# Kernel tuning notes

Measured on AMD Instinct MI355X. Metric: run time of the kernel, lower is better.

## Reference

```python
import jax, jax.numpy as jnp
import numpy as np

EMBED_DIM = 1024
NUM_HEADS = 16
HEAD_DIM = EMBED_DIM // NUM_HEADS


def setup_inputs() -> dict:
    key = jax.random.key(0)
    k_x, k_wqkv, k_bqkv, k_wo, k_bo = jax.random.split(key, 5)
    B, T, C = 4, 2048, EMBED_DIM
    bound = 1.0 / np.sqrt(C)
    return {
        "x": jax.random.normal(k_x, (B, T, C), dtype=jnp.float32),
        "w_qkv": jax.random.uniform(k_wqkv, (C, 3 * C), jnp.float32, -bound, bound),
        "b_qkv": jax.random.uniform(k_bqkv, (3 * C,), jnp.float32, -bound, bound),
        "w_out": jax.random.uniform(k_wo, (C, C), jnp.float32, -bound, bound),
        "b_out": jax.random.uniform(k_bo, (C,), jnp.float32, -bound, bound),
    }


def reference(x, w_qkv, b_qkv, w_out, b_out):
    B, T, C = x.shape
    H, D = NUM_HEADS, HEAD_DIM
    qkv = x @ w_qkv + b_qkv                       # [B,T,3C]
    qkv = qkv.reshape(B, T, 3, H, D)
    q, k, v = qkv[:, :, 0], qkv[:, :, 1], qkv[:, :, 2]  # [B,T,H,D]
    scale = 1.0 / np.sqrt(D).astype(np.float32)
    scores = jnp.einsum("bqhd,bkhd->bhqk", q, k) * scale  # [B,H,T,T]
    causal = jnp.tril(jnp.ones((T, T), dtype=bool))
    scores = jnp.where(causal, scores, -jnp.inf)
    attn = jax.nn.softmax(scores, axis=-1)
    # dropout p=0.0 / eval mode -> identity
    ctx = jnp.einsum("bhqk,bkhd->bqhd", attn, v).reshape(B, T, C)
    return ctx @ w_out + b_out
```

## Files before the change

kernel.cpp:

```cpp
#include <hip/hip_runtime.h>
#include <hip/hip_bf16.h>

#define NB 4
#define NT 2048
#define NC 1024
#define NH 16
#define ND 64
#define BT (NB*NT)
#define LOG2E 1.4426950408889634f
#define NEG_BIG (-3.0e38f)
#define MLC 28.853900817779268f

typedef __attribute__((ext_vector_type(8))) short bf16x8;
typedef __attribute__((ext_vector_type(4))) float f32x4;

static __device__ __forceinline__ short f2bf(float f) {
    union { float f; unsigned u; } v; v.f = f;
    unsigned r = (v.u + 0x7fffu + ((v.u >> 16) & 1u)) >> 16;
    return (short)r;
}

static __device__ __forceinline__ unsigned pk2(float a, float b) {
#if __has_builtin(__builtin_amdgcn_cvt_pk_bf16_f32)
    auto v = __builtin_amdgcn_cvt_pk_bf16_f32(a, b);
    union { decltype(v) v; unsigned u; } c; c.v = v; return c.u;
#else
    return (unsigned)(unsigned short)f2bf(a) | ((unsigned)(unsigned short)f2bf(b) << 16);
#endif
}

static __device__ __forceinline__ f32x4 mfma16(bf16x8 a, bf16x8 b, f32x4 c) {
    return __builtin_amdgcn_mfma_f32_16x16x32_bf16(a, b, c, 0, 0, 0);
}

static __device__ __forceinline__ float fexp2(float x) {
#if __has_builtin(__builtin_amdgcn_exp2f)
    return __builtin_amdgcn_exp2f(x);
#else
    return exp2f(x);
#endif
}

template<int GOFF>
static __device__ __forceinline__ void gload_lds16(const short* g, short* l) {
    __builtin_amdgcn_global_load_lds(
        (const __attribute__((address_space(1))) void*)g,
        (__attribute__((address_space(3))) void*)l,
        16, GOFF, 0);
}

__global__ __launch_bounds__(256)
void xcvt(const float* __restrict__ x, short* __restrict__ xb)
{
    const size_t i = ((size_t)blockIdx.x * 256 + threadIdx.x) * 8;
    float4 f0 = *(const float4*)(x + i);
    float4 f1 = *(const float4*)(x + i + 4);
    uint4 p;
    p.x = pk2(f0.x, f0.y); p.y = pk2(f0.z, f0.w);
    p.z = pk2(f1.x, f1.y); p.w = pk2(f1.z, f1.w);
    *(uint4*)(xb + i) = p;
}

__global__ __launch_bounds__(256)
void transpose_w(const float* __restrict__ w, short* __restrict__ wt, int R, int Cn)
{
    __shared__ short t[64][72];
    const int tid = threadIdx.x;
    const int r0 = blockIdx.x * 64;
    const int c0 = blockIdx.y * 64;
    {
        const int rl = tid >> 2, c4 = (tid & 3) << 4;
        const float* src = w + (size_t)(r0 + rl) * Cn + c0 + c4;
        float4 f0 = *(const float4*)(src + 0);
        float4 f1 = *(const float4*)(src + 4);
        float4 f2 = *(const float4*)(src + 8);
        float4 f3 = *(const float4*)(src + 12);
        short* d = &t[rl][c4];
        d[0]=f2bf(f0.x); d[1]=f2bf(f0.y); d[2]=f2bf(f0.z); d[3]=f2bf(f0.w);
        d[4]=f2bf(f1.x); d[5]=f2bf(f1.y); d[6]=f2bf(f1.z); d[7]=f2bf(f1.w);
        d[8]=f2bf(f2.x); d[9]=f2bf(f2.y); d[10]=f2bf(f2.z); d[11]=f2bf(f2.w);
        d[12]=f2bf(f3.x); d[13]=f2bf(f3.y); d[14]=f2bf(f3.z); d[15]=f2bf(f3.w);
    }
    __syncthreads();
    {
        const int cl = tid >> 2, r4 = (tid & 3) << 4;
        bf16x8 p0, p1;
#pragma unroll
        for (int j = 0; j < 8; ++j) { p0[j] = t[r4 + j][cl]; p1[j] = t[r4 + 8 + j][cl]; }
        short* dst = wt + (size_t)(c0 + cl) * R + r0 + r4;
        *(bf16x8*)dst       = p0;
        *(bf16x8*)(dst + 8) = p1;
    }
}

__global__ __launch_bounds__(256)
void qkv_gemm(const short* __restrict__ xb, const short* __restrict__ wt,
              const float* __restrict__ bias,
              short* __restrict__ q, short* __restrict__ k, short* __restrict__ vt)
{
    __shared__ short aLds[128 * 64];
    __shared__ short bLds[128 * 64];
    const int tid  = threadIdx.x;
    const int lane = tid & 63;
    const int wave = tid >> 6;
    const int waveM = wave & 1;
    const int waveN = wave >> 1;
    const int quad = lane >> 4;
    const int l15  = lane & 15;
    const int l7   = l15 & 7;
    const int m0 = blockIdx.x * 128;
    const int n0 = blockIdx.y * 128;

    const int rsub   = lane >> 3;
    const int cchunk = (lane & 7) ^ rsub;
    const int gcol   = cchunk * 8;

    f32x4 acc[4][4];
#pragma unroll
    for (int i = 0; i < 4; ++i)
#pragma unroll
        for (int j = 0; j < 4; ++j) acc[i][j] = 0.0f;

    for (int k0 = 0; k0 < NC; k0 += 64) {
#pragma unroll
        for (int i = 0; i < 4; ++i) {
            const int rbase = wave * 32 + i * 8;
            gload_lds16<0>(xb + (size_t)(m0 + rbase + rsub) * NC + k0 + gcol,
                           &aLds[rbase * 64]);
        }
#pragma unroll
        for (int i = 0; i < 4; ++i) {
            const int rbase = wave * 32 + i * 8;
            gload_lds16<0>(wt + (size_t)(n0 + rbase + rsub) * NC + k0 + gcol,
                           &bLds[rbase * 64]);
        }
        __syncthreads();

#pragma unroll
        for (int kd = 0; kd < 2; ++kd) {
            bf16x8 af[4], bfr[4];
#pragma unroll
            for (int mi = 0; mi < 4; ++mi) {
                const int r = waveM*64 + mi*16 + l15;
                af[mi] = *(const bf16x8*)&aLds[r*64 + (((kd*4 + quad) ^ l7) * 8)];
            }
#pragma unroll
            for (int ni = 0; ni < 4; ++ni) {
                const int r = waveN*64 + ni*16 + l15;
                bfr[ni] = *(const bf16x8*)&bLds[r*64 + (((kd*4 + quad) ^ l7) * 8)];
            }
#pragma unroll
            for (int mi = 0; mi < 4; ++mi)
#pragma unroll
                for (int ni = 0; ni < 4; ++ni)
                    acc[mi][ni] = mfma16(af[mi], bfr[ni], acc[mi][ni]);
        }
        __syncthreads();
    }

#pragma unroll
    for (int mi = 0; mi < 4; ++mi) {
#pragma unroll
        for (int ni = 0; ni < 4; ++ni) {
            const int n = n0 + waveN*64 + ni*16 + l15;
            const float bb = bias[n];
            const int s = n >> 10;
            const int h = (n >> 6) & 15;
            const int d = n & 63;
#pragma unroll
            for (int r = 0; r < 4; ++r) {
                const int m = m0 + waveM*64 + mi*16 + quad*4 + r;
                const int b = m >> 11;
                const int t = m & (NT - 1);
                const float val = acc[mi][ni][r] + bb;
                const size_t bhx = (size_t)(b * NH + h);
                if (s == 0)      q [(bhx * NT + t) * ND + d] = f2bf(val * 0.125f);
                else if (s == 1) k [(bhx * NT + t) * ND + d] = f2bf(val);
                else             vt[(bhx * ND + d) * NT + t] = f2bf(val);
            }
        }
    }
}

__global__ __launch_bounds__(256)
void attn(const short* __restrict__ q, const short* __restrict__ k,
          const short* __restrict__ vt, short* __restrict__ ctx)
{
    __shared__ short kbuf[2][64 * 64];
    __shared__ short vbuf[2][64 * 64];
    __shared__ short pbuf[4][32 * 64];
    const int tid  = threadIdx.x;
    const int lane = tid & 63;
    const int wave = tid >> 6;
    const int quad = lane >> 4;
    const int l15  = lane & 15;
    const int l7   = l15 & 7;
    const int bh = blockIdx.x;
    const int b  = bh >> 4;
    const int h  = bh & 15;

    const short* Qp = q  + (size_t)bh * NT * ND;
    const short* Kp = k  + (size_t)bh * NT * ND;
    const short* Vp = vt + (size_t)bh * ND * NT;

    const int srow   = lane >> 3;
    const int schunk = ((lane & 7) ^ srow) * 8;
    short* pw = &pbuf[wave][0];

    for (int half = 0; half < 2; ++half) {
        const int qblock = half ? (15 - (int)blockIdx.y) : (int)blockIdx.y;
        const int qb  = qblock * 128;
        const int wq0 = qb + wave * 32;
        const int ktB = 2 * qblock + 2;

        bf16x8 qf[2][2];
#pragma unroll
        for (int mi = 0; mi < 2; ++mi)
#pragma unroll
            for (int kd = 0; kd < 2; ++kd)
                qf[mi][kd] = *(const bf16x8*)(Qp + (size_t)(wq0 + mi*16 + l15) * ND + kd*32 + quad*8);

        f32x4 ot[4][2];
        f32x4 lv[2];
#pragma unroll
        for (int di = 0; di < 4; ++di)
#pragma unroll
            for (int mi = 0; mi < 2; ++mi) ot[di][mi] = 0.0f;
        lv[0] = 0.0f; lv[1] = 0.0f;

        {
            const short* Ks = Kp + (size_t)(wave*16 + srow) * ND + schunk;
            gload_lds16<0>(Ks,          &kbuf[0][(wave*16    ) * 64]);
            gload_lds16<0>(Ks + 8*ND,   &kbuf[0][(wave*16 + 8) * 64]);
            const short* Vs = Vp + (size_t)(wave*16 + srow) * NT + schunk;
            gload_lds16<0>(Vs,          &vbuf[0][(wave*16    ) * 64]);
            gload_lds16<0>(Vs + 8*NT,   &vbuf[0][(wave*16 + 8) * 64]);
        }

        for (int kt = 0; kt < ktB; ++kt) {
            const int p  = kt & 1;
            const int kb = kt << 6;
            __syncthreads();

            if (kt + 1 < ktB) {
                const int kb2 = kb + 64;
                const short* Ks = Kp + (size_t)(kb2 + wave*16 + srow) * ND + schunk;
                gload_lds16<0>(Ks,        &kbuf[1-p][(wave*16    ) * 64]);
                gload_lds16<0>(Ks + 8*ND, &kbuf[1-p][(wave*16 + 8) * 64]);
                const short* Vs = Vp + (size_t)(wave*16 + srow) * NT + kb2 + schunk;
                gload_lds16<0>(Vs,        &vbuf[1-p][(wave*16    ) * 64]);
                gload_lds16<0>(Vs + 8*NT, &vbuf[1-p][(wave*16 + 8) * 64]);
            }

            if (kb > wq0 + 31) continue;

            bf16x8 kf[4][2];
#pragma unroll
            for (int ni = 0; ni < 4; ++ni)
#pragma unroll
                for (int kd = 0; kd < 2; ++kd)
                    kf[ni][kd] = *(const bf16x8*)
                        &kbuf[p][(ni*16 + l15)*64 + (((kd*4 + quad) ^ l7) * 8)];

            f32x4 st[4][2];
#pragma unroll
            for (int ni = 0; ni < 4; ++ni)
#pragma unroll
                for (int mi = 0; mi < 2; ++mi) {
                    st[ni][mi] = 0.0f;
                    st[ni][mi] = mfma16(kf[ni][0], qf[mi][0], st[ni][mi]);
                    st[ni][mi] = mfma16(kf[ni][1], qf[mi][1], st[ni][mi]);
                }

            if (kb + 63 > wq0) {
#pragma unroll
                for (int ni = 0; ni < 4; ++ni)
#pragma unroll
                    for (int mi = 0; mi < 2; ++mi) {
                        const int qrow = wq0 + mi*16 + l15;
#pragma unroll
                        for (int r = 0; r < 4; ++r) {
                            const int key = kb + ni*16 + quad*4 + r;
                            if (key > qrow) st[ni][mi][r] = NEG_BIG;
                        }
                    }
            }

#pragma unroll
            for (int mi = 0; mi < 2; ++mi) {
#pragma unroll
                for (int ni = 0; ni < 4; ++ni) {
#pragma unroll
                    for (int r = 0; r < 4; ++r)
                        st[ni][mi][r] = fexp2(fmaf(st[ni][mi][r], LOG2E, -MLC));
                    lv[mi] += st[ni][mi];
                    const f32x4 v = st[ni][mi];
                    *(uint2*)&pw[(mi*16 + l15)*64
                                 + (((2*ni + (quad >> 1)) ^ l7) * 8)
                                 + (quad & 1) * 4] =
                        make_uint2(pk2(v[0], v[1]), pk2(v[2], v[3]));
                }
            }

            bf16x8 vf[4][2], pf[2][2];
#pragma unroll
            for (int di = 0; di < 4; ++di)
#pragma unroll
                for (int kd = 0; kd < 2; ++kd)
                    vf[di][kd] = *(const bf16x8*)
                        &vbuf[p][(di*16 + l15)*64 + (((kd*4 + quad) ^ l7) * 8)];
#pragma unroll
            for (int mi = 0; mi < 2; ++mi)
#pragma unroll
                for (int kd = 0; kd < 2; ++kd)
                    pf[mi][kd] = *(const bf16x8*)
                        &pw[(mi*16 + l15)*64 + (((kd*4 + quad) ^ l7) * 8)];

#pragma unroll
            for (int di = 0; di < 4; ++di)
#pragma unroll
                for (int mi = 0; mi < 2; ++mi) {
                    ot[di][mi] = mfma16(vf[di][0], pf[mi][0], ot[di][mi]);
                    ot[di][mi] = mfma16(vf[di][1], pf[mi][1], ot[di][mi]);
                }
        }

#pragma unroll
        for (int mi = 0; mi < 2; ++mi) {
            float l = lv[mi][0] + lv[mi][1] + lv[mi][2] + lv[mi][3];
            l += __shfl_xor(l, 16);
            l += __shfl_xor(l, 32);
            const float inv = 1.0f / l;
            const int t = wq0 + mi*16 + l15;
            short* dst = ctx + ((size_t)(b * NT + t)) * NC + h*64 + quad*4;
#pragma unroll
            for (int di = 0; di < 4; ++di) {
                const f32x4 v = ot[di][mi] * inv;
                *(uint2*)(dst + di*16) = make_uint2(pk2(v[0], v[1]), pk2(v[2], v[3]));
            }
        }
        __syncthreads();
    }
}

__global__ __launch_bounds__(256)
void out_gemm(const short* __restrict__ a, const short* __restrict__ wt,
              const float* __restrict__ bias, float* __restrict__ out)
{
    __shared__ short aLds[128 * 64];
    __shared__ short bLds[128 * 64];
    const int tid  = threadIdx.x;
    const int lane = tid & 63;
    const int wave = tid >> 6;
    const int waveM = wave & 1;
    const int waveN = wave >> 1;
    const int quad = lane >> 4;
    const int l15  = lane & 15;
    const int l7   = l15 & 7;
    const int m0 = blockIdx.x * 128;
    const int n0 = blockIdx.y * 128;

    const int rsub   = lane >> 3;
    const int cchunk = (lane & 7) ^ rsub;
    const int gcol   = cchunk * 8;

    f32x4 acc[4][4];
#pragma unroll
    for (int i = 0; i < 4; ++i)
#pragma unroll
        for (int j = 0; j < 4; ++j) acc[i][j] = 0.0f;

    for (int k0 = 0; k0 < NC; k0 += 64) {
#pragma unroll
        for (int i = 0; i < 4; ++i) {
            const int rbase = wave * 32 + i * 8;
            gload_lds16<0>(a + (size_t)(m0 + rbase + rsub) * NC + k0 + gcol,
                           &aLds[rbase * 64]);
        }
#pragma unroll
        for (int i = 0; i < 4; ++i) {
            const int rbase = wave * 32 + i * 8;
            gload_lds16<0>(wt + (size_t)(n0 + rbase + rsub) * NC + k0 + gcol,
                           &bLds[rbase * 64]);
        }
        __syncthreads();

#pragma unroll
        for (int kd = 0; kd < 2; ++kd) {
            bf16x8 af[4], bfr[4];
#pragma unroll
            for (int mi = 0; mi < 4; ++mi) {
                const int r = waveM*64 + mi*16 + l15;
                af[mi] = *(const bf16x8*)&aLds[r*64 + (((kd*4 + quad) ^ l7) * 8)];
            }
#pragma unroll
            for (int ni = 0; ni < 4; ++ni) {
                const int r = waveN*64 + ni*16 + l15;
                bfr[ni] = *(const bf16x8*)&bLds[r*64 + (((kd*4 + quad) ^ l7) * 8)];
            }
#pragma unroll
            for (int mi = 0; mi < 4; ++mi)
#pragma unroll
                for (int ni = 0; ni < 4; ++ni)
                    acc[mi][ni] = mfma16(af[mi], bfr[ni], acc[mi][ni]);
        }
        __syncthreads();
    }

#pragma unroll
    for (int mi = 0; mi < 4; ++mi) {
#pragma unroll
        for (int ni = 0; ni < 4; ++ni) {
            const int n = n0 + waveN*64 + ni*16 + l15;
            const float bb = bias[n];
#pragma unroll
            for (int r = 0; r < 4; ++r) {
                const int m = m0 + waveM*64 + mi*16 + quad*4 + r;
                out[(size_t)m * NC + n] = acc[mi][ni][r] + bb;
            }
        }
    }
}

extern "C" void kernel_launch(void* const* d_in, const int* in_sizes, int n_in,
                              void* d_out, int out_size, void* d_ws, size_t ws_size,
                              hipStream_t stream)
{
    const float* x     = (const float*)d_in[0];
    const float* w_qkv = (const float*)d_in[1];
    const float* b_qkv = (const float*)d_in[2];
    const float* w_out = (const float*)d_in[3];
    const float* b_out = (const float*)d_in[4];
    float* out = (float*)d_out;

    const size_t SZ = (size_t)NB * NH * NT * ND;
    short* q   = (short*)d_ws;
    short* kk  = q  + SZ;
    short* vt  = kk + SZ;
    short* ctx = vt + SZ;
    short* xbf = ctx + SZ;
    short* wTq = ctx;
    short* wTo = xbf;

    hipLaunchKernelGGL(xcvt, dim3(BT*NC/(256*8)), dim3(256), 0, stream, x, xbf);
    hipLaunchKernelGGL(transpose_w, dim3(16, 48), dim3(256), 0, stream,
                       w_qkv, wTq, NC, 3*NC);
    hipLaunchKernelGGL(qkv_gemm, dim3(BT/128, (3*NC)/128), dim3(256), 0, stream,
                       xbf, wTq, b_qkv, q, kk, vt);
    hipLaunchKernelGGL(attn, dim3(NB*NH, 8), dim3(256), 0, stream,
                       q, kk, vt, ctx);
    hipLaunchKernelGGL(transpose_w, dim3(16, 16), dim3(256), 0, stream,
                       w_out, wTo, NC, NC);
    hipLaunchKernelGGL(out_gemm, dim3(BT/128, NC/128), dim3(256), 0, stream,
                       ctx, wTo, b_out, out);
}
```

Baseline: 276.4 us.

## Rewrite QKV GEMM as 256x256 tile, 8-wave double-buffered pipelined kernel

Replaces the 128x128, 4-wave QKV projection GEMM with a 256x256 tile kernel using 8 waves and double-buffered LDS. Global-to-LDS loads for the next k-tiles are interleaved with quarter-tile MFMA phases, using explicit waitcnt, barriers and s_setprio to overlap memory traffic with compute. The goal is higher data reuse per block and hidden load latency. In exchange it uses much more LDS (128 KB) and more accumulator registers, which limits occupancy, and the hand-placed waitcnt and barrier scheduling is fragile.

```diff
diff --git a/kernel.cpp b/kernel.cpp
--- a/kernel.cpp
+++ b/kernel.cpp
@@ -93,13 +93,13 @@
     }
 }
 
-__global__ __launch_bounds__(256)
-void qkv_gemm(const short* __restrict__ xb, const short* __restrict__ wt,
-              const float* __restrict__ bias,
-              short* __restrict__ q, short* __restrict__ k, short* __restrict__ vt)
+__global__ __launch_bounds__(512, 2)
+void qkv_gemm8(const short* __restrict__ xb, const short* __restrict__ wt,
+               const float* __restrict__ bias,
+               short* __restrict__ q, short* __restrict__ k, short* __restrict__ vt)
 {
-    __shared__ short aLds[128 * 64];
-    __shared__ short bLds[128 * 64];
+    __shared__ short aLds[2][256 * 64];
+    __shared__ short bLds[2][256 * 64];
     const int tid  = threadIdx.x;
     const int lane = tid & 63;
     const int wave = tid >> 6;
@@ -108,58 +108,109 @@
     const int quad = lane >> 4;
     const int l15  = lane & 15;
     const int l7   = l15 & 7;
-    const int m0 = blockIdx.x * 128;
-    const int n0 = blockIdx.y * 128;
-
-    const int rsub   = lane >> 3;
-    const int cchunk = (lane & 7) ^ rsub;
-    const int gcol   = cchunk * 8;
-
-    f32x4 acc[4][4];
-#pragma unroll
-    for (int i = 0; i < 4; ++i)
+    const int m0 = blockIdx.x * 256;
+    const int n0 = blockIdx.y * 256;
+
+    const int rsub = lane >> 3;
+    const int gcol = ((lane & 7) ^ rsub) * 8;
+
+    f32x4 acc[8][4];
+#pragma unroll
+    for (int i = 0; i < 8; ++i)
 #pragma unroll
         for (int j = 0; j < 4; ++j) acc[i][j] = 0.0f;
 
-    for (int k0 = 0; k0 < NC; k0 += 64) {
-#pragma unroll
-        for (int i = 0; i < 4; ++i) {
-            const int rbase = wave * 32 + i * 8;
-            gload_lds16<0>(xb + (size_t)(m0 + rbase + rsub) * NC + k0 + gcol,
-                           &aLds[rbase * 64]);
-        }
-#pragma unroll
-        for (int i = 0; i < 4; ++i) {
-            const int rbase = wave * 32 + i * 8;
-            gload_lds16<0>(wt + (size_t)(n0 + rbase + rsub) * NC + k0 + gcol,
-                           &bLds[rbase * 64]);
-        }
-        __syncthreads();
-
-#pragma unroll
-        for (int kd = 0; kd < 2; ++kd) {
-            bf16x8 af[4], bfr[4];
-#pragma unroll
-            for (int mi = 0; mi < 4; ++mi) {
-                const int r = waveM*64 + mi*16 + l15;
-                af[mi] = *(const bf16x8*)&aLds[r*64 + (((kd*4 + quad) ^ l7) * 8)];
-            }
-#pragma unroll
-            for (int ni = 0; ni < 4; ++ni) {
-                const int r = waveN*64 + ni*16 + l15;
-                bfr[ni] = *(const bf16x8*)&bLds[r*64 + (((kd*4 + quad) ^ l7) * 8)];
-            }
-#pragma unroll
-            for (int mi = 0; mi < 4; ++mi)
-#pragma unroll
-                for (int ni = 0; ni < 4; ++ni)
-                    acc[mi][ni] = mfma16(af[mi], bfr[ni], acc[mi][ni]);
-        }
-        __syncthreads();
-    }
-
-#pragma unroll
-    for (int mi = 0; mi < 4; ++mi) {
+    bf16x8 aF[4][2];
+    bf16x8 bF[2][2][2];
+
+    auto stA = [&](int p, int kt, int h) {
+#pragma unroll
+        for (int i = 0; i < 2; ++i) {
+            const int rb = h*128 + i*64 + wave*8;
+            gload_lds16<0>(xb + (size_t)(m0 + rb + rsub) * NC + kt*64 + gcol,
+                           &aLds[p][rb * 64]);
+        }
+    };
+    auto stB = [&](int p, int kt, int h) {
+#pragma unroll
+        for (int i = 0; i < 2; ++i) {
+            const int rb = h*128 + i*64 + wave*8;
+            gload_lds16<0>(wt + (size_t)(n0 + rb + rsub) * NC + kt*64 + gcol,
+                           &bLds[p][rb * 64]);
+        }
+    };
+    auto rdA = [&](int p, int mh) {
+#pragma unroll
+        for (int mi = 0; mi < 4; ++mi)
+#pragma unroll
+            for (int kd = 0; kd < 2; ++kd) {
+                const int r = waveM*128 + mh*64 + mi*16 + l15;
+                aF[mi][kd] = *(const bf16x8*)
+                    &aLds[p][r*64 + (((kd*4 + quad) ^ l7) * 8)];
+            }
+    };
+    auto rdB = [&](int p, int nh) {
+#pragma unroll
+        for (int ni = 0; ni < 2; ++ni)
+#pragma unroll
+            for (int kd = 0; kd < 2; ++kd) {
+                const int r = waveN*64 + nh*32 + ni*16 + l15;
+                bF[nh][ni][kd] = *(const bf16x8*)
+                    &bLds[p][r*64 + (((kd*4 + quad) ^ l7) * 8)];
+            }
+    };
+    auto mmQ = [&](int mh, int nh) {
+        __builtin_amdgcn_s_setprio(1);
+#pragma unroll
+        for (int mi = 0; mi < 4; ++mi)
+#pragma unroll
+            for (int ni = 0; ni < 2; ++ni) {
+                f32x4 c = acc[mh*4 + mi][nh*2 + ni];
+                c = mfma16(aF[mi][0], bF[nh][ni][0], c);
+                c = mfma16(aF[mi][1], bF[nh][ni][1], c);
+                acc[mh*4 + mi][nh*2 + ni] = c;
+            }
+        __builtin_amdgcn_s_setprio(0);
+    };
+
+    stB(0, 0, 0); stB(0, 0, 1);
+    stA(0, 0, 0); stA(0, 0, 1);
+    stB(1, 1, 0); stB(1, 1, 1);
+    asm volatile("s_waitcnt vmcnt(4)" ::: "memory");
+    __builtin_amdgcn_s_barrier();
+
+#pragma unroll 1
+    for (int kt = 0; kt < 16; ++kt) {
+        const int p = kt & 1;
+        rdA(p, 0); rdB(p, 0);
+        if (kt + 1 < 16) stA(p ^ 1, kt + 1, 0);
+        asm volatile("s_waitcnt lgkmcnt(8)" ::: "memory");
+        __builtin_amdgcn_s_barrier();
+        asm volatile("s_waitcnt lgkmcnt(0)" ::: "memory");
+        mmQ(0, 0);
+        __builtin_amdgcn_s_barrier();
+        rdB(p, 1);
+        if (kt + 1 < 16) stA(p ^ 1, kt + 1, 1);
+        __builtin_amdgcn_s_barrier();
+        asm volatile("s_waitcnt lgkmcnt(0)" ::: "memory");
+        mmQ(0, 1);
+        __builtin_amdgcn_s_barrier();
+        rdA(p, 1);
+        if (kt + 2 < 16) stB(p, kt + 2, 0);
+        __builtin_amdgcn_s_barrier();
+        asm volatile("s_waitcnt lgkmcnt(0)" ::: "memory");
+        mmQ(1, 1);
+        __builtin_amdgcn_s_barrier();
+        if (kt + 2 < 16) stB(p, kt + 2, 1);
+        __builtin_amdgcn_s_barrier();
+        mmQ(1, 0);
+        if (kt + 2 < 16)      asm volatile("s_waitcnt vmcnt(4)" ::: "memory");
+        else if (kt + 1 < 16) asm volatile("s_waitcnt vmcnt(0)" ::: "memory");
+        __builtin_amdgcn_s_barrier();
+    }
+
+#pragma unroll
+    for (int mi = 0; mi < 8; ++mi) {
 #pragma unroll
         for (int ni = 0; ni < 4; ++ni) {
             const int n = n0 + waveN*64 + ni*16 + l15;
@@ -169,7 +220,7 @@
             const int d = n & 63;
 #pragma unroll
             for (int r = 0; r < 4; ++r) {
-                const int m = m0 + waveM*64 + mi*16 + quad*4 + r;
+                const int m = m0 + waveM*128 + mi*16 + quad*4 + r;
                 const int b = m >> 11;
                 const int t = m & (NT - 1);
                 const float val = acc[mi][ni][r] + bb;
@@ -445,7 +496,7 @@
     hipLaunchKernelGGL(xcvt, dim3(BT*NC/(256*8)), dim3(256), 0, stream, x, xbf);
     hipLaunchKernelGGL(transpose_w, dim3(16, 48), dim3(256), 0, stream,
                        w_qkv, wTq, NC, 3*NC);
-    hipLaunchKernelGGL(qkv_gemm, dim3(BT/128, (3*NC)/128), dim3(256), 0, stream,
+    hipLaunchKernelGGL(qkv_gemm8, dim3(BT/256, (3*NC)/256), dim3(512), 0, stream,
                        xbf, wTq, b_qkv, q, kk, vt);
     hipLaunchKernelGGL(attn, dim3(NB*NH, 8), dim3(256), 0, stream,
                        q, kk, vt, ctx);
```

New measurement: 285.4 us. 3.3% more time.
